# Optimization experiments

Measured on AMD Instinct MI355X. Metric: run time of the kernel, lower is better.

## Reference

```python
import jax, jax.numpy as jnp
import numpy as np

FUZZY_FACTOR = 2
REG_WT = 0.0008


def setup_inputs() -> dict:
    key = jax.random.key(0)
    k1, k2 = jax.random.split(key)
    logits = jax.random.normal(k1, (2, 4, 128, 128, 128), dtype=jnp.float32)
    y_pred = jax.nn.softmax(logits, axis=1)  # module assumes softmax already applied
    image = jax.random.normal(k2, (2, 1, 128, 128, 128), dtype=jnp.float32)
    return {"y_pred": y_pred, "image": image}


def _neighbor_sum(x):
    # x: [B, K, D, H, W]; 3x3x3 ones kernel with zero center, SAME padding,
    # applied independently per (batch, cluster) channel.
    B, K, D, H, W = x.shape
    kernel = jnp.ones((1, 1, 3, 3, 3), x.dtype).at[0, 0, 1, 1, 1].set(0.0)
    y = jax.lax.conv_general_dilated(
        x.reshape(B * K, 1, D, H, W), kernel,
        window_strides=(1, 1, 1), padding="SAME",
        dimension_numbers=("NCDHW", "OIDHW", "NCDHW"))
    return y.reshape(B, K, D, H, W)


def reference(y_pred, image):
    B, K = y_pred.shape[0], y_pred.shape[1]
    N = int(np.prod(y_pred.shape[2:]))
    pred = y_pred.reshape(B, K, N)          # [B, K, N]
    img = image.reshape(B, N)               # [B, N]

    mem = pred ** FUZZY_FACTOR              # fuzzy memberships [B, K, N]

    # cluster centroids v_k = sum(img*mem)/sum(mem)  -> [B, K]
    v = jnp.sum(img[:, None, :] * mem, axis=2) / jnp.sum(mem, axis=2)

    # J_1 = sum_i mem_i * (img - v_i)^2   -> [B, N]
    J1 = jnp.sum(mem * (img[:, None, :] - v[:, :, None]) ** 2, axis=1)

    # neighbor sum of each cluster's membership map (box filter minus center)
    nb = _neighbor_sum(mem.reshape(y_pred.shape)).reshape(B, K, N)
    # sum over j != i, computed once as total - self (identical algebra)
    J_in = jnp.sum(nb, axis=1, keepdims=True) - nb  # [B, K, N]
    J2 = jnp.sum(mem * J_in, axis=1)                # [B, N]

    return jnp.mean(J1) + REG_WT * jnp.mean(J2)
```

## Files before the change

kernel.cpp:

```cpp
#include <hip/hip_runtime.h>


#define BB 2
#define KK 4
#define DD 128
#define HH 128
#define WW 128
#define PLANE (HH * WW)
#define SD 8
#define NBD (DD / SD)
#define HR 8
#define NBH (HH / HR)
#define NT 256
#define SLROW 128
#define SLICE (KK * 4 * SLROW)

typedef const void __attribute__((address_space(1))) gvoid_t;
typedef void __attribute__((address_space(3))) svoid_t;
#define GLD(gp, lp) __builtin_amdgcn_global_load_lds((gvoid_t*)(gp), (svoid_t*)(lp), 16, 0, 0)
#define WAIT_VM0() __builtin_amdgcn_s_waitcnt(0x0F70)

__global__ __launch_bounds__(NT) void rfcm_main(
    const float* __restrict__ yp, const float* __restrict__ img,
    double* __restrict__ ws)
{
    __shared__ __align__(16) float sbuf[4 * 2 * SLICE];

    const int tid = threadIdx.x;
    const int wv  = tid >> 6;
    const int L   = tid & 63;
    const int wl  = L & 31;
    const int hy  = L >> 5;
    const int c0  = wl << 2;

    const int bid  = blockIdx.x;
    const int xcd  = bid & 7;
    const int idx  = bid >> 3;
    const int sl   = idx >> 4;
    const int ht   = idx & 15;
    const int slab = sl * 8 + xcd;
    const int b    = slab >> 4;
    const int dsb  = slab & 15;

    const int h0  = ht * HR;
    const int hp0 = h0 + (wv << 1);
    const int h   = hp0 + hy;
    const int d0  = dsb * SD;

    float* const mybuf = &sbuf[wv * 2 * SLICE];

    const int rr = L >> 5;
    const int cl = (L & 31) << 2;

    auto dma_batch = [&](int t) {
        if ((unsigned)t >= (unsigned)DD) return;
        float* const bb = mybuf + (t & 1) * SLICE;
        #pragma unroll
        for (int k = 0; k < KK; k++) {
            const float* pb = yp + (size_t)((b * KK + k) * DD + t) * PLANE;
            #pragma unroll
            for (int rp = 0; rp < 2; rp++) {
                int g = hp0 - 1 + (rp << 1) + rr;
                g = g < 0 ? 0 : (g > HH - 1 ? HH - 1 : g);
                const float* gp = pb + g * WW + cl;
                float* lp = bb + (k * 4 + (rp << 1)) * SLROW;
                GLD(gp, lp);
            }
        }
    };

    const bool okL = (wl > 0), okR = (wl < 31);
    const float msc = (h > 0)      ? 1.f : 0.f;
    const float psc = (h < HH - 1) ? 1.f : 0.f;

    auto extract = [&](int t, int k, float4& s9, float4& mm) {
        const float* p3 = mybuf + (t & 1) * SLICE + (k * 4 + hy) * SLROW + c0;
        const float4 a4 = *(const float4*)(p3);
        const float4 b4 = *(const float4*)(p3 + SLROW);
        const float4 c4 = *(const float4*)(p3 + 2 * SLROW);
        const float4 sb = make_float4(b4.x*b4.x, b4.y*b4.y, b4.z*b4.z, b4.w*b4.w);
        mm = sb;
        float4 v;
        v.x = fmaf(a4.x*a4.x, msc, fmaf(c4.x*c4.x, psc, sb.x));
        v.y = fmaf(a4.y*a4.y, msc, fmaf(c4.y*c4.y, psc, sb.y));
        v.z = fmaf(a4.z*a4.z, msc, fmaf(c4.z*c4.z, psc, sb.z));
        v.w = fmaf(a4.w*a4.w, msc, fmaf(c4.w*c4.w, psc, sb.w));
        const float vL = okL ? __shfl_up(v.w, 1)   : 0.f;
        const float vR = okR ? __shfl_down(v.x, 1) : 0.f;
        s9.x = vL  + v.x + v.y;
        s9.y = v.x + v.y + v.z;
        s9.z = v.y + v.z + v.w;
        s9.w = v.z + v.w + vR;
    };

    const float* imgb = img + (size_t)b * DD * PLANE + h * WW + c0;

    dma_batch(d0 - 1);
    dma_batch(d0);
    float4 iv = *(const float4*)(imgb + (size_t)d0 * PLANE);
    WAIT_VM0();

    float4 s9p[KK], s9c[KK], mc[KK], dum;
    const bool vprev = (d0 > 0);
    #pragma unroll
    for (int k = 0; k < KK; k++) {
        if (vprev) extract(d0 - 1, k, s9p[k], dum);
        else       s9p[k] = make_float4(0.f, 0.f, 0.f, 0.f);
        extract(d0, k, s9c[k], mc[k]);
    }
    dma_batch(d0 + 1);

    float smf[KK] = {0,0,0,0}, sif[KK] = {0,0,0,0}, saf[KK] = {0,0,0,0};
    float j2f = 0.f;

    #pragma unroll 2
    for (int i = 0; i < SD; i++) {
        const int d = d0 + i;
        WAIT_VM0();

        float4 ivn = iv;
        if (i < SD - 1) ivn = *(const float4*)(imgb + (size_t)(d + 1) * PLANE);
        if (i <= SD - 2) dma_batch(d + 2);
        const bool vn = (d + 1 < DD);
        const float4 iv2 = make_float4(iv.x*iv.x, iv.y*iv.y, iv.z*iv.z, iv.w*iv.w);

        float4 summ  = make_float4(0.f, 0.f, 0.f, 0.f);
        float4 sumbk = make_float4(0.f, 0.f, 0.f, 0.f);
        float4 cross = make_float4(0.f, 0.f, 0.f, 0.f);

        #pragma unroll
        for (int k = 0; k < KK; k++) {
            float4 s9n, mn;
            if (vn) extract(d + 1, k, s9n, mn);
            else { s9n = make_float4(0.f,0.f,0.f,0.f); mn = s9n; }

            const float4 m = mc[k];
            float4 bk;
            bk.x = s9p[k].x + s9c[k].x + s9n.x;
            bk.y = s9p[k].y + s9c[k].y + s9n.y;
            bk.z = s9p[k].z + s9c[k].z + s9n.z;
            bk.w = s9p[k].w + s9c[k].w + s9n.w;

            summ.x += m.x; summ.y += m.y; summ.z += m.z; summ.w += m.w;
            sumbk.x += bk.x; sumbk.y += bk.y; sumbk.z += bk.z; sumbk.w += bk.w;
            cross.x = fmaf(m.x, bk.x - m.x, cross.x);
            cross.y = fmaf(m.y, bk.y - m.y, cross.y);
            cross.z = fmaf(m.z, bk.z - m.z, cross.z);
            cross.w = fmaf(m.w, bk.w - m.w, cross.w);

            smf[k] += (m.x + m.y) + (m.z + m.w);
            sif[k] = fmaf(m.x, iv.x,  fmaf(m.y, iv.y,  fmaf(m.z, iv.z,  fmaf(m.w, iv.w,  sif[k]))));
            saf[k] = fmaf(m.x, iv2.x, fmaf(m.y, iv2.y, fmaf(m.z, iv2.z, fmaf(m.w, iv2.w, saf[k]))));

            s9p[k] = s9c[k]; s9c[k] = s9n; mc[k] = mn;
        }

        j2f += (summ.x * (sumbk.x - summ.x) - cross.x)
             + (summ.y * (sumbk.y - summ.y) - cross.y)
             + (summ.z * (sumbk.z - summ.z) - cross.z)
             + (summ.w * (sumbk.w - summ.w) - cross.w);

        iv = ivn;
    }

    double q[13];
    #pragma unroll
    for (int k = 0; k < KK; k++) {
        q[k] = (double)smf[k]; q[4 + k] = (double)sif[k]; q[8 + k] = (double)saf[k];
    }
    q[12] = (double)j2f;

    #pragma unroll
    for (int qq = 0; qq < 13; qq++) {
        double v = q[qq];
        #pragma unroll
        for (int off = 32; off > 0; off >>= 1) v += __shfl_down(v, off, 64);
        q[qq] = v;
    }

    __syncthreads();
    double* red = (double*)sbuf;
    const int lane = tid & 63, wid = tid >> 6;
    if (lane == 0) {
        #pragma unroll
        for (int qq = 0; qq < 13; qq++) red[wid * 13 + qq] = q[qq];
    }
    __syncthreads();
    if (tid < 13) {
        const double sfin = red[tid] + red[13 + tid] + red[26 + tid] + red[39 + tid];
        int idxo;
        if      (tid < 4)  idxo = b * KK + tid;
        else if (tid < 8)  idxo = 8  + b * KK + (tid - 4);
        else if (tid < 12) idxo = 16 + b * KK + (tid - 8);
        else               idxo = 24;
        unsafeAtomicAdd(&ws[idxo], sfin);
    }
}

__global__ void rfcm_fin(const double* __restrict__ ws, float* __restrict__ out)
{
    if (threadIdx.x == 0 && blockIdx.x == 0) {
        double j1 = 0;
        #pragma unroll
        for (int i = 0; i < BB * KK; i++)
            j1 += ws[16 + i] - ws[8 + i] * ws[8 + i] / ws[i];
        const double invBN = 1.0 / ((double)BB * (double)DD * (double)HH * (double)WW);
        out[0] = (float)(j1 * invBN + 0.0008 * ws[24] * invBN);
    }
}

extern "C" void kernel_launch(void* const* d_in, const int* in_sizes, int n_in,
                              void* d_out, int out_size, void* d_ws, size_t ws_size,
                              hipStream_t stream) {
    const float* yp  = (const float*)d_in[0];
    const float* img = (const float*)d_in[1];
    float* out = (float*)d_out;
    double* ws = (double*)d_ws;

    hipMemsetAsync(d_ws, 0, 25 * sizeof(double), stream);

    dim3 grid(BB * NBD * NBH);
    rfcm_main<<<grid, NT, 0, stream>>>(yp, img, ws);
    rfcm_fin<<<1, 64, 0, stream>>>(ws, out);
}
```

Before: 123.4 us.

## Replace LDS DMA staging with direct register loads and cross-lane halo sharing

Drops the global_load_lds double-buffered shared-memory staging and loads each wave's own row plus one halo row straight into registers, ping-ponging two register plane buffers. The middle vertical neighbour comes from the partner half-wave through a shfl_xor instead of being re-read from LDS. The depth slab is halved, so the grid doubles and occupancy rises, at the cost of more halo-plane reloads and no explicit vmcnt wait control. It also removes the large LDS footprint and the block-wide barrier before the reduction.

```diff
diff --git a/kernel.cpp b/kernel.cpp
--- a/kernel.cpp
+++ b/kernel.cpp
@@ -7,24 +7,17 @@
 #define HH 128
 #define WW 128
 #define PLANE (HH * WW)
-#define SD 8
+#define SD 4
 #define NBD (DD / SD)
 #define HR 8
 #define NBH (HH / HR)
 #define NT 256
-#define SLROW 128
-#define SLICE (KK * 4 * SLROW)
-
-typedef const void __attribute__((address_space(1))) gvoid_t;
-typedef void __attribute__((address_space(3))) svoid_t;
-#define GLD(gp, lp) __builtin_amdgcn_global_load_lds((gvoid_t*)(gp), (svoid_t*)(lp), 16, 0, 0)
-#define WAIT_VM0() __builtin_amdgcn_s_waitcnt(0x0F70)
 
 __global__ __launch_bounds__(NT) void rfcm_main(
     const float* __restrict__ yp, const float* __restrict__ img,
     double* __restrict__ ws)
 {
-    __shared__ __align__(16) float sbuf[4 * 2 * SLICE];
+    __shared__ double red[4 * 13];
 
     const int tid = threadIdx.x;
     const int wv  = tid >> 6;
@@ -39,52 +32,50 @@
     const int sl   = idx >> 4;
     const int ht   = idx & 15;
     const int slab = sl * 8 + xcd;
-    const int b    = slab >> 4;
-    const int dsb  = slab & 15;
+    const int b    = slab >> 5;
+    const int dsb  = slab & 31;
 
     const int h0  = ht * HR;
     const int hp0 = h0 + (wv << 1);
     const int h   = hp0 + hy;
     const int d0  = dsb * SD;
 
-    float* const mybuf = &sbuf[wv * 2 * SLICE];
-
-    const int rr = L >> 5;
-    const int cl = (L & 31) << 2;
-
-    auto dma_batch = [&](int t) {
-        if ((unsigned)t >= (unsigned)DD) return;
-        float* const bb = mybuf + (t & 1) * SLICE;
+    const int gHr = (hy == 0) ? (hp0 - 1) : (hp0 + 2);
+    const int gH  = gHr < 0 ? 0 : (gHr > HH - 1 ? HH - 1 : gHr);
+    const float hsc = (gHr >= 0 && gHr <= HH - 1) ? 1.f : 0.f;
+
+    const bool okL = (wl > 0), okR = (wl < 31);
+
+    const float* pO[KK];
+    const long dH = (long)(gH - h) * WW;
+    #pragma unroll
+    for (int k = 0; k < KK; k++)
+        pO[k] = yp + (size_t)((b * KK + k) * DD) * PLANE + (size_t)h * WW + c0;
+
+    float4 oA[KK], aA[KK], oB[KK], aB[KK];
+
+    auto lplane = [&](int t, float4* o, float4* a) {
+        const size_t off = (size_t)t * PLANE;
         #pragma unroll
         for (int k = 0; k < KK; k++) {
-            const float* pb = yp + (size_t)((b * KK + k) * DD + t) * PLANE;
-            #pragma unroll
-            for (int rp = 0; rp < 2; rp++) {
-                int g = hp0 - 1 + (rp << 1) + rr;
-                g = g < 0 ? 0 : (g > HH - 1 ? HH - 1 : g);
-                const float* gp = pb + g * WW + cl;
-                float* lp = bb + (k * 4 + (rp << 1)) * SLROW;
-                GLD(gp, lp);
-            }
+            o[k] = *(const float4*)(pO[k] + off);
+            a[k] = *(const float4*)(pO[k] + off + dH);
         }
     };
 
-    const bool okL = (wl > 0), okR = (wl < 31);
-    const float msc = (h > 0)      ? 1.f : 0.f;
-    const float psc = (h < HH - 1) ? 1.f : 0.f;
-
-    auto extract = [&](int t, int k, float4& s9, float4& mm) {
-        const float* p3 = mybuf + (t & 1) * SLICE + (k * 4 + hy) * SLROW + c0;
-        const float4 a4 = *(const float4*)(p3);
-        const float4 b4 = *(const float4*)(p3 + SLROW);
-        const float4 c4 = *(const float4*)(p3 + 2 * SLROW);
-        const float4 sb = make_float4(b4.x*b4.x, b4.y*b4.y, b4.z*b4.z, b4.w*b4.w);
-        mm = sb;
+    auto extract = [&](const float4 o4, const float4 a4, float4& s9, float4& mm) {
+        const float4 m = make_float4(o4.x*o4.x, o4.y*o4.y, o4.z*o4.z, o4.w*o4.w);
+        mm = m;
+        float4 p;
+        p.x = __shfl_xor(m.x, 32, 64);
+        p.y = __shfl_xor(m.y, 32, 64);
+        p.z = __shfl_xor(m.z, 32, 64);
+        p.w = __shfl_xor(m.w, 32, 64);
         float4 v;
-        v.x = fmaf(a4.x*a4.x, msc, fmaf(c4.x*c4.x, psc, sb.x));
-        v.y = fmaf(a4.y*a4.y, msc, fmaf(c4.y*c4.y, psc, sb.y));
-        v.z = fmaf(a4.z*a4.z, msc, fmaf(c4.z*c4.z, psc, sb.z));
-        v.w = fmaf(a4.w*a4.w, msc, fmaf(c4.w*c4.w, psc, sb.w));
+        v.x = fmaf(a4.x*a4.x, hsc, m.x + p.x);
+        v.y = fmaf(a4.y*a4.y, hsc, m.y + p.y);
+        v.z = fmaf(a4.z*a4.z, hsc, m.z + p.z);
+        v.w = fmaf(a4.w*a4.w, hsc, m.w + p.w);
         const float vL = okL ? __shfl_up(v.w, 1)   : 0.f;
         const float vR = okR ? __shfl_down(v.x, 1) : 0.f;
         s9.x = vL  + v.x + v.y;
@@ -93,37 +84,35 @@
         s9.w = v.z + v.w + vR;
     };
 
-    const float* imgb = img + (size_t)b * DD * PLANE + h * WW + c0;
-
-    dma_batch(d0 - 1);
-    dma_batch(d0);
+    const float* imgb = img + (size_t)b * DD * PLANE + (size_t)h * WW + c0;
+
+    const bool vprev = (d0 > 0);
+    lplane(vprev ? d0 - 1 : 0, oA, aA);
+    lplane(d0, oB, aB);
     float4 iv = *(const float4*)(imgb + (size_t)d0 * PLANE);
-    WAIT_VM0();
 
     float4 s9p[KK], s9c[KK], mc[KK], dum;
-    const bool vprev = (d0 > 0);
-    #pragma unroll
-    for (int k = 0; k < KK; k++) {
-        if (vprev) extract(d0 - 1, k, s9p[k], dum);
-        else       s9p[k] = make_float4(0.f, 0.f, 0.f, 0.f);
-        extract(d0, k, s9c[k], mc[k]);
-    }
-    dma_batch(d0 + 1);
+    #pragma unroll
+    for (int k = 0; k < KK; k++) extract(oA[k], aA[k], s9p[k], dum);
+    if (!vprev) {
+        #pragma unroll
+        for (int k = 0; k < KK; k++) s9p[k] = make_float4(0.f, 0.f, 0.f, 0.f);
+    }
+    lplane(d0 + 1, oA, aA);
+    #pragma unroll
+    for (int k = 0; k < KK; k++) extract(oB[k], aB[k], s9c[k], mc[k]);
 
     float smf[KK] = {0,0,0,0}, sif[KK] = {0,0,0,0}, saf[KK] = {0,0,0,0};
     float j2f = 0.f;
 
-    #pragma unroll 2
-    for (int i = 0; i < SD; i++) {
+    auto step = [&](int i, float4* oC, float4* aC, float4* oP, float4* aP) {
         const int d = d0 + i;
-        WAIT_VM0();
-
+        const bool vn = (d + 1 < DD);
         float4 ivn = iv;
-        if (i < SD - 1) ivn = *(const float4*)(imgb + (size_t)(d + 1) * PLANE);
-        if (i <= SD - 2) dma_batch(d + 2);
-        const bool vn = (d + 1 < DD);
+        if (vn) ivn = *(const float4*)(imgb + (size_t)(d + 1) * PLANE);
+        if (i < SD - 1 && d + 2 < DD) lplane(d + 2, oP, aP);
+
         const float4 iv2 = make_float4(iv.x*iv.x, iv.y*iv.y, iv.z*iv.z, iv.w*iv.w);
-
         float4 summ  = make_float4(0.f, 0.f, 0.f, 0.f);
         float4 sumbk = make_float4(0.f, 0.f, 0.f, 0.f);
         float4 cross = make_float4(0.f, 0.f, 0.f, 0.f);
@@ -131,7 +120,7 @@
         #pragma unroll
         for (int k = 0; k < KK; k++) {
             float4 s9n, mn;
-            if (vn) extract(d + 1, k, s9n, mn);
+            if (vn) extract(oC[k], aC[k], s9n, mn);
             else { s9n = make_float4(0.f,0.f,0.f,0.f); mn = s9n; }
 
             const float4 m = mc[k];
@@ -161,6 +150,12 @@
              + (summ.w * (sumbk.w - summ.w) - cross.w);
 
         iv = ivn;
+    };
+
+    #pragma unroll
+    for (int ii = 0; ii < SD / 2; ii++) {
+        step(2 * ii,     oA, aA, oB, aB);
+        step(2 * ii + 1, oB, aB, oA, aA);
     }
 
     double q[13];
@@ -178,8 +173,6 @@
         q[qq] = v;
     }
 
-    __syncthreads();
-    double* red = (double*)sbuf;
     const int lane = tid & 63, wid = tid >> 6;
     if (lane == 0) {
         #pragma unroll
```

Measured after the change: 134.3 us. +8.8%, slower.
